# Performance work log

Hardware: AMD Instinct MI355X
Metric: run time of the kernel (lower is better)

Reference implementation:

```python
import jax, jax.numpy as jnp
import numpy as np

NEG = 0.01  # leaky_relu negative slope

def leaky(x):
    return jax.nn.leaky_relu(x, NEG)

def mlp3(x, W0, b0, W1, b1, W2, b2):
    h = leaky(x @ W0 + b0)
    h = leaky(h @ W1 + b1)
    return h @ W2 + b2

B_, T_, N_FINE, F_IN = 2, 4, 64800, 78
N_COARSE, E_LAT, H, D_OUT = 842, 5894, 256, 256

def setup_inputs() -> dict:
    key = jax.random.key(0)
    ks = jax.random.split(key, 24)
    def lin(k, i, o):
        return jax.random.normal(k, (i, o), jnp.float32) * 0.02, jnp.zeros((o,), jnp.float32)
    x = jax.random.normal(ks[0], (B_, T_, N_FINE, F_IN), jnp.float32)
    # one edge per fine node: src = node index, dst = its coarse h3 cell
    edge_index = jnp.stack([jnp.arange(N_FINE, dtype=jnp.int32),
                            jax.random.randint(ks[1], (N_FINE,), 0, N_COARSE, dtype=jnp.int32)])
    edge_attr = 2.0 * jax.random.uniform(ks[2], (N_FINE, 2), jnp.float32) - 1.0  # [sin d, cos d]
    latent_edge_index = jax.random.randint(ks[3], (2, E_LAT), 0, N_COARSE, dtype=jnp.int32)
    latent_edge_attr = 2.0 * jax.random.uniform(ks[4], (E_LAT, 2), jnp.float32) - 1.0
    h3_nodes = jax.random.normal(ks[5], (N_COARSE, F_IN), jnp.float32) * 0.02
    eW0, eb0 = lin(ks[6], 2 * F_IN + 2, H); eW1, eb1 = lin(ks[7], H, H); eW2, eb2 = lin(ks[8], H, D_OUT)
    nW0, nb0 = lin(ks[9], F_IN + D_OUT, H); nW1, nb1 = lin(ks[10], H, H); nW2, nb2 = lin(ks[11], H, D_OUT)
    rW0, rb0 = lin(ks[12], 2, H); rW1, rb1 = lin(ks[13], H, H); rW2, rb2 = lin(ks[14], H, D_OUT)
    rWs, rbs = lin(ks[15], 2, D_OUT)
    return dict(x=x, edge_index=edge_index, edge_attr=edge_attr,
                latent_edge_index=latent_edge_index, latent_edge_attr=latent_edge_attr,
                h3_nodes=h3_nodes,
                eW0=eW0, eb0=eb0, eW1=eW1, eb1=eb1, eW2=eW2, eb2=eb2,
                nW0=nW0, nb0=nb0, nW1=nW1, nb1=nb1, nW2=nW2, nb2=nb2,
                rW0=rW0, rb0=rb0, rW1=rW1, rb1=rb1, rW2=rW2, rb2=rb2,
                rWs=rWs, rbs=rbs)

def reference(x, edge_index, edge_attr, latent_edge_index, latent_edge_attr, h3_nodes,
              eW0, eb0, eW1, eb1, eW2, eb2,
              nW0, nb0, nW1, nb1, nW2, nb2,
              rW0, rb0, rW1, rb1, rW2, rb2, rWs, rbs):
    b, t, n, f = x.shape
    B = b * t
    xf = x.reshape(B, n, f)                      # (b t) n f
    src, dst = edge_index[0], edge_index[1]      # [E]
    nc = h3_nodes.shape[0]
    E = src.shape[0]
    # --- edge MLP: gather src fine feats, dst latent feats, edge attrs ---
    e_in = jnp.concatenate([
        xf[:, src],                                          # [B,E,f]
        jnp.broadcast_to(h3_nodes[dst][None], (B, E, f)),    # [B,E,f]
        jnp.broadcast_to(edge_attr[None], (B, E, 2)),        # [B,E,2]
    ], axis=-1)
    msgs = mlp3(e_in, eW0, eb0, eW1, eb1, eW2, eb2)          # [B,E,D]
    # --- scatter-sum to coarse nodes ---
    agg = jax.vmap(lambda m: jax.ops.segment_sum(m, dst, num_segments=nc))(msgs)  # [B,nc,D]
    # --- node MLP on concat(latent nodes, aggregated messages) ---
    n_in = jnp.concatenate([jnp.broadcast_to(h3_nodes[None], (B, nc, f)), agg], axis=-1)
    nodes = mlp3(n_in, nW0, nb0, nW1, nb1, nW2, nb2)          # [B,nc,D]
    nodes = nodes.reshape(b, t, nc, -1)
    # --- residual MLP over latent edge attrs (eval: dropout off, parametrized skip) ---
    h = leaky(latent_edge_attr @ rW0 + rb0)
    h = leaky(h @ rW1 + rb1)
    attrs = h @ rW2 + rb2 + (latent_edge_attr @ rWs + rbs)
    return (nodes, latent_edge_index, attrs)
```

## Files before the change

### kernel.cpp

```cpp
#include <hip/hip_runtime.h>

#define E_EDGES 64800
#define NC      842
#define NB      8
#define FIN     78
#define E_LAT   5894
#define NROWS_NODE (NB*NC)
#define NTILES_E 2025

#define OUT_IDX_OFF   1724416
#define OUT_IDX_N     11788
#define OUT_ATTR_OFF  1736204

#define AGG_OFF    0
#define CNT_OFF    6897664
#define CUR_OFF    6901032
#define SSRC_OFF   6904400
#define SDST_OFF   7163600
#define SATTR_OFF  7293200
#define WPACK_OFF  7811600

#define WOFF_E0 0
#define WOFF_E1 40960
#define WOFF_E2 106496
#define WOFF_N0 172032
#define WOFF_N1 262144
#define WOFF_N2 327680
#define WOFF_R0 393216
#define WOFF_R1 401408
#define WOFF_R2 466944

#define SH   262
#define SA_N 362

typedef __bf16 bf16x8 __attribute__((ext_vector_type(8)));
typedef float  f32x4  __attribute__((ext_vector_type(4)));

__device__ __forceinline__ unsigned short f2bf(float f) {
    unsigned u = __builtin_bit_cast(unsigned, f);
    return (unsigned short)((u + 0x7fffu + ((u >> 16) & 1u)) >> 16);
}
__device__ __forceinline__ unsigned packRTZ(float lo, float hi) {
    return __builtin_amdgcn_perm(__builtin_bit_cast(unsigned, hi),
                                 __builtin_bit_cast(unsigned, lo), 0x07060302u);
}

template<int MF>
__device__ __forceinline__ void zero_acc(f32x4 (&acc)[MF][4]) {
#pragma unroll
    for (int mf = 0; mf < MF; ++mf)
#pragma unroll
        for (int nf = 0; nf < 4; ++nf)
            acc[mf][nf] = (f32x4){0.f, 0.f, 0.f, 0.f};
}

template<int MF, int NKS>
__device__ __forceinline__ void run_layer(const unsigned short* lA, int strideA,
                                          const unsigned short* Wp, int nfg0,
                                          int m15, int q, f32x4 (&acc)[MF][4]) {
    const unsigned short* wp0 = Wp + (size_t)nfg0 * 512 + (threadIdx.x & 63) * 8;
    bf16x8 bcur[4], bnxt[4];
#pragma unroll
    for (int nf = 0; nf < 4; ++nf) bcur[nf] = *(const bf16x8*)(wp0 + nf * 512);
#pragma unroll
    for (int kk = 0; kk < NKS; ++kk) {
        if (kk + 1 < NKS) {
#pragma unroll
            for (int nf = 0; nf < 4; ++nf)
                bnxt[nf] = *(const bf16x8*)(wp0 + (size_t)(kk + 1) * 16 * 512 + nf * 512);
        }
        bf16x8 a[MF];
#pragma unroll
        for (int mf = 0; mf < MF; ++mf)
            a[mf] = *(const bf16x8*)(lA + (mf * 16 + m15) * strideA + kk * 32 + q * 8);
#pragma unroll
        for (int nf = 0; nf < 4; ++nf)
#pragma unroll
            for (int mf = 0; mf < MF; ++mf)
                acc[mf][nf] = __builtin_amdgcn_mfma_f32_16x16x32_bf16(a[mf], bcur[nf], acc[mf][nf], 0, 0, 0);
#pragma unroll
        for (int nf = 0; nf < 4; ++nf) bcur[nf] = bnxt[nf];
    }
}

template<int MF>
__device__ __forceinline__ void epi_act(unsigned short* Sb, int stride, const f32x4 (&acc)[MF][4],
                                        const float* bias, int w, int m15, int q) {
#pragma unroll
    for (int nf = 0; nf < 4; ++nf) {
        int col = w * 64 + nf * 16 + m15;
        float bv = bias[col];
#pragma unroll
        for (int mf = 0; mf < MF; ++mf)
#pragma unroll
            for (int r4 = 0; r4 < 4; ++r4) {
                int row = mf * 16 + q * 4 + r4;
                float y = acc[mf][nf][r4] + bv;
                y = fmaxf(y, 0.01f * y);
                Sb[row * stride + col] = (unsigned short)(__builtin_bit_cast(unsigned, y) >> 16);
            }
    }
}

__global__ void pack_weights(const float* s0, const float* s1, const float* s2,
                             const float* s3, const float* s4, const float* s5,
                             const float* s6, const float* s7, const float* s8,
                             unsigned short* wp) {
    const int ksA[9]  = {5, 8, 8, 11, 8, 8, 1, 8, 8};
    const int kaA[9]  = {158, 256, 256, 334, 256, 256, 2, 256, 256};
    const int offA[9] = {WOFF_E0, WOFF_E1, WOFF_E2, WOFF_N0, WOFF_N1, WOFF_N2,
                         WOFF_R0, WOFF_R1, WOFF_R2};
    const float* srcs[9] = {s0, s1, s2, s3, s4, s5, s6, s7, s8};
    int rem = blockIdx.x;
    int l = 0;
    while (rem >= ksA[l] * 16) { rem -= ksA[l] * 16; ++l; }
    int kk = rem >> 4, nf = rem & 15;
    int lane = threadIdx.x >> 3, j = threadIdx.x & 7;
    int k = kk * 32 + (lane >> 4) * 8 + j;
    int n = nf * 16 + (lane & 15);
    float v = (k < kaA[l]) ? srcs[l][k * 256 + n] : 0.f;
    wp[(size_t)offA[l] + (size_t)(kk * 16 + nf) * 512 + lane * 8 + j] = f2bf(v);
}

__global__ void hist_kernel(const int* __restrict__ dstA, int* __restrict__ cnt) {
    int e = blockIdx.x * 256 + threadIdx.x;
    if (e < E_EDGES) atomicAdd(&cnt[dstA[e]], 1);
}
__global__ void scan_kernel(const int* __restrict__ cnt, int* __restrict__ cursor) {
    __shared__ int s[1024];
    int t = threadIdx.x;
    s[t] = (t < NC) ? cnt[t] : 0;
    __syncthreads();
    for (int d = 1; d < 1024; d <<= 1) {
        int v = (t >= d) ? s[t - d] : 0;
        __syncthreads();
        s[t] += v;
        __syncthreads();
    }
    if (t < NC) cursor[t] = (t == 0) ? 0 : s[t - 1];
}
__global__ void scatter_kernel(const int* __restrict__ srcA, const int* __restrict__ dstA,
                               const float* __restrict__ eattr, int* __restrict__ cursor,
                               int* __restrict__ ssrc, short* __restrict__ sdst,
                               float2* __restrict__ sattr) {
    int e = blockIdx.x * 256 + threadIdx.x;
    if (e < E_EDGES) {
        int d = dstA[e];
        int p = atomicAdd(&cursor[d], 1);
        ssrc[p] = srcA[e];
        sdst[p] = (short)d;
        sattr[p] = ((const float2*)eattr)[e];
    }
}

__global__ __launch_bounds__(256, 6) void edge_mlp_kernel(
    const float* __restrict__ x, const float* __restrict__ h3,
    const float* __restrict__ eb0, const float* __restrict__ eb1, const float* __restrict__ eb2,
    const unsigned short* __restrict__ wpack, const int* __restrict__ ssrc,
    const short* __restrict__ sdst, const float2* __restrict__ sattr,
    float* __restrict__ agg) {
    __shared__ __align__(16) unsigned short S[32 * SH];
    __shared__ short dstl[32];
    __shared__ unsigned char starts[36];
    __shared__ int nseg;

    const int base = blockIdx.x * 32, b = blockIdx.y;
    const int tid = threadIdx.x, lane = tid & 63, w = tid >> 6;
    const int m15 = lane & 15, q = lane >> 4;

    if (tid < 32) dstl[tid] = sdst[base + tid];
    __syncthreads();

    if (tid == 0) {
        int ns = 0; short prev = -2;
        for (int r = 0; r < 32; ++r) {
            short d = dstl[r];
            if (d != prev) { starts[ns++] = (unsigned char)r; prev = d; }
        }
        starts[ns] = 32;
        nseg = ns;
    }

    {
        const int rr = tid >> 3, j = tid & 7;
        const int eg = base + rr;
        const float* xr = x + ((size_t)b * E_EDGES + ssrc[eg]) * FIN;
        const float* hr = h3 + (int)dstl[rr] * FIN;
        unsigned short* Sr = S + rr * SH;
#pragma unroll
        for (int t = 0; t < 5; ++t) {
            int p = j + 8 * t;
            if (p < 39) {
                float2 f = *(const float2*)(xr + 2 * p);
                float2 g = *(const float2*)(hr + 2 * p);
                *(unsigned*)(Sr + 2 * p) = packRTZ(f.x, f.y);
                *(unsigned*)(Sr + 78 + 2 * p) = packRTZ(g.x, g.y);
            } else if (p == 39) {
                float2 a2 = sattr[eg];
                *(unsigned*)(Sr + 156) = packRTZ(a2.x, a2.y);
                *(unsigned*)(Sr + 158) = 0;
            }
        }
    }
    float bnf[4];
#pragma unroll
    for (int nf = 0; nf < 4; ++nf) bnf[nf] = eb2[w * 64 + nf * 16 + m15];
    __syncthreads();

    f32x4 acc[2][4];
    zero_acc<2>(acc);
    run_layer<2, 5>(S, SH, wpack + WOFF_E0, w * 4, m15, q, acc);
    __syncthreads();
    epi_act<2>(S, SH, acc, eb0, w, m15, q);
    __syncthreads();

    zero_acc<2>(acc);
    run_layer<2, 8>(S, SH, wpack + WOFF_E1, w * 4, m15, q, acc);
    __syncthreads();
    epi_act<2>(S, SH, acc, eb1, w, m15, q);
    __syncthreads();

    zero_acc<2>(acc);
    run_layer<2, 8>(S, SH, wpack + WOFF_E2, w * 4, m15, q, acc);

    const int ns = nseg;
#pragma unroll
    for (int nf = 0; nf < 4; ++nf) {
        for (int s = 0; s < ns; ++s) {
            const int lo = starts[s], hi = starts[s + 1];
            float t = 0.f;
#pragma unroll
            for (int mf = 0; mf < 2; ++mf)
#pragma unroll
                for (int r4 = 0; r4 < 4; ++r4) {
                    int row = mf * 16 + q * 4 + r4;
                    t += (row >= lo && row < hi) ? acc[mf][nf][r4] : 0.f;
                }
            t += __shfl_xor(t, 16, 64);
            t += __shfl_xor(t, 32, 64);
            if (q == nf) {
                int dc = dstl[lo];
                atomicAdd(&agg[((size_t)b * NC + dc) * 256 + w * 64 + nf * 16 + m15],
                          t + bnf[nf] * (float)(hi - lo));
            }
        }
    }
}

__global__ __launch_bounds__(256, 4) void node_mlp_kernel(
    const float* __restrict__ h3, const float* __restrict__ agg,
    const float* __restrict__ nb0, const float* __restrict__ nb1, const float* __restrict__ nb2,
    const unsigned short* __restrict__ wpack, float* __restrict__ out) {
    __shared__ __align__(16) unsigned short S[16 * SA_N];

    const int base = blockIdx.x * 16;
    const int tid = threadIdx.x, lane = tid & 63, w = tid >> 6;
    const int m15 = lane & 15, q = lane >> 4;

    {
        const int rr = tid >> 4, l16 = tid & 15;
        const int jj = base + rr;
        const int vl = jj < NROWS_NODE;
        const int c = vl ? jj % NC : 0;
        const float* hr = h3 + c * FIN;
        const float* ar = agg + (size_t)jj * 256;
        unsigned short* Sr = S + rr * SA_N;
#pragma unroll
        for (int t = 0; t < 12; ++t) {
            int p = l16 + 16 * t;
            if (p < 39) {
                float2 f = *(const float2*)(hr + 2 * p);
                *(unsigned*)(Sr + 2 * p) = packRTZ(f.x, f.y);
            } else if (p < 167) {
                unsigned v = 0;
                if (vl) { float2 f = *(const float2*)(ar + 2 * p - 78); v = packRTZ(f.x, f.y); }
                *(unsigned*)(Sr + 2 * p) = v;
            } else if (p < 176) {
                *(unsigned*)(Sr + 2 * p) = 0;
            }
        }
    }
    __syncthreads();

    f32x4 acc[1][4];
    zero_acc<1>(acc);
    run_layer<1, 11>(S, SA_N, wpack + WOFF_N0, w * 4, m15, q, acc);
    __syncthreads();
    epi_act<1>(S, SA_N, acc, nb0, w, m15, q);
    __syncthreads();

    zero_acc<1>(acc);
    run_layer<1, 8>(S, SA_N, wpack + WOFF_N1, w * 4, m15, q, acc);
    __syncthreads();
    epi_act<1>(S, SA_N, acc, nb1, w, m15, q);
    __syncthreads();

    zero_acc<1>(acc);
    run_layer<1, 8>(S, SA_N, wpack + WOFF_N2, w * 4, m15, q, acc);

#pragma unroll
    for (int nf = 0; nf < 4; ++nf) {
        int col = w * 64 + nf * 16 + m15;
        float bv = nb2[col];
#pragma unroll
        for (int r4 = 0; r4 < 4; ++r4) {
            int jj = base + q * 4 + r4;
            if (jj < NROWS_NODE) out[(size_t)jj * 256 + col] = acc[0][nf][r4] + bv;
        }
    }
}

__global__ __launch_bounds__(256, 4) void tail_kernel(
    const float* __restrict__ la, const float* __restrict__ rb0, const float* __restrict__ rb1,
    const float* __restrict__ rb2, const float* __restrict__ rWs, const float* __restrict__ rbs,
    const unsigned short* __restrict__ wpack, const int* __restrict__ lei,
    float* __restrict__ out) {
    __shared__ __align__(16) unsigned short S[32 * SH];

    const int blk = blockIdx.x;
    const int tid = threadIdx.x;
    if (blk >= 185) {
        for (int i = (blk - 185) * 256 + tid; i < OUT_IDX_N; i += 7 * 256)
            out[OUT_IDX_OFF + i] = (float)lei[i];
        return;
    }

    const int base = blk * 32;
    const int lane = tid & 63, w = tid >> 6;
    const int m15 = lane & 15, q = lane >> 4;

    {
        const int rr = tid >> 3, j = tid & 7;
        unsigned short* Sr = S + rr * SH;
        unsigned v0 = 0;
        if (j == 0 && base + rr < E_LAT) {
            float2 f = *(const float2*)(la + (size_t)(base + rr) * 2);
            v0 = packRTZ(f.x, f.y);
        }
        *(unsigned*)(Sr + 2 * j) = v0;
        *(unsigned*)(Sr + 2 * (j + 8)) = 0;
    }
    __syncthreads();

    f32x4 acc[2][4];
    zero_acc<2>(acc);
    run_layer<2, 1>(S, SH, wpack + WOFF_R0, w * 4, m15, q, acc);
    __syncthreads();
    epi_act<2>(S, SH, acc, rb0, w, m15, q);
    __syncthreads();

    zero_acc<2>(acc);
    run_layer<2, 8>(S, SH, wpack + WOFF_R1, w * 4, m15, q, acc);
    __syncthreads();
    epi_act<2>(S, SH, acc, rb1, w, m15, q);
    __syncthreads();

    zero_acc<2>(acc);
    run_layer<2, 8>(S, SH, wpack + WOFF_R2, w * 4, m15, q, acc);

    float* outA = out + OUT_ATTR_OFF;
#pragma unroll
    for (int nf = 0; nf < 4; ++nf) {
        int col = w * 64 + nf * 16 + m15;
        float bv = rb2[col] + rbs[col];
        float ws0 = rWs[col], ws1 = rWs[256 + col];
#pragma unroll
        for (int mf = 0; mf < 2; ++mf)
#pragma unroll
            for (int r4 = 0; r4 < 4; ++r4) {
                int row = mf * 16 + q * 4 + r4;
                int e = base + row;
                if (e < E_LAT) {
                    float v = acc[mf][nf][r4] + bv + la[e * 2] * ws0 + la[e * 2 + 1] * ws1;
                    outA[(size_t)e * 256 + col] = v;
                }
            }
    }
}

extern "C" void kernel_launch(void* const* d_in, const int* in_sizes, int n_in,
                              void* d_out, int out_size, void* d_ws, size_t ws_size,
                              hipStream_t stream) {
    const float* x      = (const float*)d_in[0];
    const int*   eidx   = (const int*)d_in[1];
    const float* eattr  = (const float*)d_in[2];
    const int*   lei    = (const int*)d_in[3];
    const float* la     = (const float*)d_in[4];
    const float* h3     = (const float*)d_in[5];
    const float* eW0 = (const float*)d_in[6],  *eb0 = (const float*)d_in[7];
    const float* eW1 = (const float*)d_in[8],  *eb1 = (const float*)d_in[9];
    const float* eW2 = (const float*)d_in[10], *eb2 = (const float*)d_in[11];
    const float* nW0 = (const float*)d_in[12], *nb0 = (const float*)d_in[13];
    const float* nW1 = (const float*)d_in[14], *nb1 = (const float*)d_in[15];
    const float* nW2 = (const float*)d_in[16], *nb2 = (const float*)d_in[17];
    const float* rW0 = (const float*)d_in[18], *rb0 = (const float*)d_in[19];
    const float* rW1 = (const float*)d_in[20], *rb1 = (const float*)d_in[21];
    const float* rW2 = (const float*)d_in[22], *rb2 = (const float*)d_in[23];
    const float* rWs = (const float*)d_in[24], *rbs = (const float*)d_in[25];

    char* ws = (char*)d_ws;
    float* agg    = (float*)(ws + AGG_OFF);
    int* cnt      = (int*)(ws + CNT_OFF);
    int* cur      = (int*)(ws + CUR_OFF);
    int* ssrc     = (int*)(ws + SSRC_OFF);
    short* sdst   = (short*)(ws + SDST_OFF);
    float2* sattr = (float2*)(ws + SATTR_OFF);
    unsigned short* wpack = (unsigned short*)(ws + WPACK_OFF);

    float* out = (float*)d_out;

    hipMemsetAsync(d_ws, 0, CUR_OFF, stream);

    pack_weights<<<1040, 512, 0, stream>>>(eW0, eW1, eW2, nW0, nW1, nW2, rW0, rW1, rW2, wpack);
    hist_kernel<<<254, 256, 0, stream>>>(eidx + E_EDGES, cnt);
    scan_kernel<<<1, 1024, 0, stream>>>(cnt, cur);
    scatter_kernel<<<254, 256, 0, stream>>>(eidx, eidx + E_EDGES, eattr, cur,
                                            ssrc, sdst, sattr);
    tail_kernel<<<192, 256, 0, stream>>>(la, rb0, rb1, rb2, rWs, rbs, wpack, lei, out);
    edge_mlp_kernel<<<dim3(NTILES_E, NB), 256, 0, stream>>>(x, h3, eb0, eb1, eb2,
                                                            wpack, ssrc, sdst, sattr, agg);
    node_mlp_kernel<<<421, 256, 0, stream>>>(h3, agg, nb0, nb1, nb2, wpack, out);
}
```

Baseline: 689.8 us.

## Merge sort passes into one block and fold tail MLP into edge kernel

Replaces the histogram, scan and scatter kernels with one single-block kernel that builds the counting sort in shared memory. The residual latent-edge MLP and the index copy now run as extra blocks of the edge MLP grid, with launch bounds raised from 6 to 8 blocks per CU. This cuts kernel launches and the memset of the count buffers, but the counting sort now runs serially on one CU over all 64800 edges. The extra tail blocks launch for every batch slice and most exit at once, and the tighter launch bounds may cause register spills in the edge MLP.

```diff
diff --git a/kernel.cpp b/kernel.cpp
--- a/kernel.cpp
+++ b/kernel.cpp
@@ -7,6 +7,7 @@
 #define E_LAT   5894
 #define NROWS_NODE (NB*NC)
 #define NTILES_E 2025
+#define TAIL_B   192
 
 #define OUT_IDX_OFF   1724416
 #define OUT_IDX_N     11788
@@ -122,51 +123,112 @@
     wp[(size_t)offA[l] + (size_t)(kk * 16 + nf) * 512 + lane * 8 + j] = f2bf(v);
 }
 
-__global__ void hist_kernel(const int* __restrict__ dstA, int* __restrict__ cnt) {
-    int e = blockIdx.x * 256 + threadIdx.x;
-    if (e < E_EDGES) atomicAdd(&cnt[dstA[e]], 1);
-}
-__global__ void scan_kernel(const int* __restrict__ cnt, int* __restrict__ cursor) {
-    __shared__ int s[1024];
-    int t = threadIdx.x;
-    s[t] = (t < NC) ? cnt[t] : 0;
+__global__ __launch_bounds__(1024) void sort_kernel(
+    const int* __restrict__ srcA, const int* __restrict__ dstA,
+    const float* __restrict__ eattr, int* __restrict__ ssrc,
+    short* __restrict__ sdst, float2* __restrict__ sattr) {
+    __shared__ int hist[1024];
+    __shared__ int cur[1024];
+    const int t = threadIdx.x;
+    hist[t] = 0;
+    __syncthreads();
+    for (int e = t; e < E_EDGES; e += 1024) atomicAdd(&hist[dstA[e]], 1);
     __syncthreads();
     for (int d = 1; d < 1024; d <<= 1) {
-        int v = (t >= d) ? s[t - d] : 0;
-        __syncthreads();
-        s[t] += v;
-        __syncthreads();
-    }
-    if (t < NC) cursor[t] = (t == 0) ? 0 : s[t - 1];
-}
-__global__ void scatter_kernel(const int* __restrict__ srcA, const int* __restrict__ dstA,
-                               const float* __restrict__ eattr, int* __restrict__ cursor,
-                               int* __restrict__ ssrc, short* __restrict__ sdst,
-                               float2* __restrict__ sattr) {
-    int e = blockIdx.x * 256 + threadIdx.x;
-    if (e < E_EDGES) {
+        int v = (t >= d) ? hist[t - d] : 0;
+        __syncthreads();
+        hist[t] += v;
+        __syncthreads();
+    }
+    cur[t] = (t == 0) ? 0 : hist[t - 1];
+    __syncthreads();
+    for (int e = t; e < E_EDGES; e += 1024) {
         int d = dstA[e];
-        int p = atomicAdd(&cursor[d], 1);
+        int p = atomicAdd(&cur[d], 1);
         ssrc[p] = srcA[e];
         sdst[p] = (short)d;
         sattr[p] = ((const float2*)eattr)[e];
     }
 }
 
-__global__ __launch_bounds__(256, 6) void edge_mlp_kernel(
+__global__ __launch_bounds__(256, 8) void edge_mlp_kernel(
     const float* __restrict__ x, const float* __restrict__ h3,
     const float* __restrict__ eb0, const float* __restrict__ eb1, const float* __restrict__ eb2,
     const unsigned short* __restrict__ wpack, const int* __restrict__ ssrc,
     const short* __restrict__ sdst, const float2* __restrict__ sattr,
-    float* __restrict__ agg) {
+    float* __restrict__ agg,
+    const float* __restrict__ la, const float* __restrict__ rb0,
+    const float* __restrict__ rb1, const float* __restrict__ rb2,
+    const float* __restrict__ rWs, const float* __restrict__ rbs,
+    const int* __restrict__ lei, float* __restrict__ out) {
     __shared__ __align__(16) unsigned short S[32 * SH];
     __shared__ short dstl[32];
     __shared__ unsigned char starts[36];
     __shared__ int nseg;
 
-    const int base = blockIdx.x * 32, b = blockIdx.y;
     const int tid = threadIdx.x, lane = tid & 63, w = tid >> 6;
     const int m15 = lane & 15, q = lane >> 4;
+
+    if (blockIdx.x >= NTILES_E) {
+        if (blockIdx.y != 0) return;
+        const int blk = blockIdx.x - NTILES_E;
+        if (blk >= 185) {
+            for (int i = (blk - 185) * 256 + tid; i < OUT_IDX_N; i += 7 * 256)
+                out[OUT_IDX_OFF + i] = (float)lei[i];
+            return;
+        }
+        const int base = blk * 32;
+        {
+            const int rr = tid >> 3, j = tid & 7;
+            unsigned short* Sr = S + rr * SH;
+            unsigned v0 = 0;
+            if (j == 0 && base + rr < E_LAT) {
+                float2 f = *(const float2*)(la + (size_t)(base + rr) * 2);
+                v0 = packRTZ(f.x, f.y);
+            }
+            *(unsigned*)(Sr + 2 * j) = v0;
+            *(unsigned*)(Sr + 2 * (j + 8)) = 0;
+        }
+        __syncthreads();
+
+        f32x4 acc[2][4];
+        zero_acc<2>(acc);
+        run_layer<2, 1>(S, SH, wpack + WOFF_R0, w * 4, m15, q, acc);
+        __syncthreads();
+        epi_act<2>(S, SH, acc, rb0, w, m15, q);
+        __syncthreads();
+
+        zero_acc<2>(acc);
+        run_layer<2, 8>(S, SH, wpack + WOFF_R1, w * 4, m15, q, acc);
+        __syncthreads();
+        epi_act<2>(S, SH, acc, rb1, w, m15, q);
+        __syncthreads();
+
+        zero_acc<2>(acc);
+        run_layer<2, 8>(S, SH, wpack + WOFF_R2, w * 4, m15, q, acc);
+
+        float* outA = out + OUT_ATTR_OFF;
+#pragma unroll
+        for (int nf = 0; nf < 4; ++nf) {
+            int col = w * 64 + nf * 16 + m15;
+            float bv = rb2[col] + rbs[col];
+            float ws0 = rWs[col], ws1 = rWs[256 + col];
+#pragma unroll
+            for (int mf = 0; mf < 2; ++mf)
+#pragma unroll
+                for (int r4 = 0; r4 < 4; ++r4) {
+                    int row = mf * 16 + q * 4 + r4;
+                    int e = base + row;
+                    if (e < E_LAT) {
+                        float v = acc[mf][nf][r4] + bv + la[e * 2] * ws0 + la[e * 2 + 1] * ws1;
+                        outA[(size_t)e * 256 + col] = v;
+                    }
+                }
+        }
+        return;
+    }
+
+    const int base = blockIdx.x * 32, b = blockIdx.y;
 
     if (tid < 32) dstl[tid] = sdst[base + tid];
     __syncthreads();
@@ -307,74 +369,6 @@
             int jj = base + q * 4 + r4;
             if (jj < NROWS_NODE) out[(size_t)jj * 256 + col] = acc[0][nf][r4] + bv;
         }
-    }
-}
-
-__global__ __launch_bounds__(256, 4) void tail_kernel(
-    const float* __restrict__ la, const float* __restrict__ rb0, const float* __restrict__ rb1,
-    const float* __restrict__ rb2, const float* __restrict__ rWs, const float* __restrict__ rbs,
-    const unsigned short* __restrict__ wpack, const int* __restrict__ lei,
-    float* __restrict__ out) {
-    __shared__ __align__(16) unsigned short S[32 * SH];
-
-    const int blk = blockIdx.x;
-    const int tid = threadIdx.x;
-    if (blk >= 185) {
-        for (int i = (blk - 185) * 256 + tid; i < OUT_IDX_N; i += 7 * 256)
-            out[OUT_IDX_OFF + i] = (float)lei[i];
-        return;
-    }
-
-    const int base = blk * 32;
-    const int lane = tid & 63, w = tid >> 6;
-    const int m15 = lane & 15, q = lane >> 4;
-
-    {
-        const int rr = tid >> 3, j = tid & 7;
-        unsigned short* Sr = S + rr * SH;
-        unsigned v0 = 0;
-        if (j == 0 && base + rr < E_LAT) {
-            float2 f = *(const float2*)(la + (size_t)(base + rr) * 2);
-            v0 = packRTZ(f.x, f.y);
-        }
-        *(unsigned*)(Sr + 2 * j) = v0;
-        *(unsigned*)(Sr + 2 * (j + 8)) = 0;
-    }
-    __syncthreads();
-
-    f32x4 acc[2][4];
-    zero_acc<2>(acc);
-    run_layer<2, 1>(S, SH, wpack + WOFF_R0, w * 4, m15, q, acc);
-    __syncthreads();
-    epi_act<2>(S, SH, acc, rb0, w, m15, q);
-    __syncthreads();
-
-    zero_acc<2>(acc);
-    run_layer<2, 8>(S, SH, wpack + WOFF_R1, w * 4, m15, q, acc);
-    __syncthreads();
-    epi_act<2>(S, SH, acc, rb1, w, m15, q);
-    __syncthreads();
-
-    zero_acc<2>(acc);
-    run_layer<2, 8>(S, SH, wpack + WOFF_R2, w * 4, m15, q, acc);
-
-    float* outA = out + OUT_ATTR_OFF;
-#pragma unroll
-    for (int nf = 0; nf < 4; ++nf) {
-        int col = w * 64 + nf * 16 + m15;
-        float bv = rb2[col] + rbs[col];
-        float ws0 = rWs[col], ws1 = rWs[256 + col];
-#pragma unroll
-        for (int mf = 0; mf < 2; ++mf)
-#pragma unroll
-            for (int r4 = 0; r4 < 4; ++r4) {
-                int row = mf * 16 + q * 4 + r4;
-                int e = base + row;
-                if (e < E_LAT) {
-                    float v = acc[mf][nf][r4] + bv + la[e * 2] * ws0 + la[e * 2 + 1] * ws1;
-                    outA[(size_t)e * 256 + col] = v;
-                }
-            }
     }
 }
 
@@ -400,8 +394,6 @@
 
     char* ws = (char*)d_ws;
     float* agg    = (float*)(ws + AGG_OFF);
-    int* cnt      = (int*)(ws + CNT_OFF);
-    int* cur      = (int*)(ws + CUR_OFF);
     int* ssrc     = (int*)(ws + SSRC_OFF);
     short* sdst   = (short*)(ws + SDST_OFF);
     float2* sattr = (float2*)(ws + SATTR_OFF);
@@ -409,15 +401,12 @@
 
     float* out = (float*)d_out;
 
-    hipMemsetAsync(d_ws, 0, CUR_OFF, stream);
+    hipMemsetAsync(d_ws, 0, CNT_OFF, stream);
 
     pack_weights<<<1040, 512, 0, stream>>>(eW0, eW1, eW2, nW0, nW1, nW2, rW0, rW1, rW2, wpack);
-    hist_kernel<<<254, 256, 0, stream>>>(eidx + E_EDGES, cnt);
-    scan_kernel<<<1, 1024, 0, stream>>>(cnt, cur);
-    scatter_kernel<<<254, 256, 0, stream>>>(eidx, eidx + E_EDGES, eattr, cur,
-                                            ssrc, sdst, sattr);
-    tail_kernel<<<192, 256, 0, stream>>>(la, rb0, rb1, rb2, rWs, rbs, wpack, lei, out);
-    edge_mlp_kernel<<<dim3(NTILES_E, NB), 256, 0, stream>>>(x, h3, eb0, eb1, eb2,
-                                                            wpack, ssrc, sdst, sattr, agg);
+    sort_kernel<<<1, 1024, 0, stream>>>(eidx, eidx + E_EDGES, eattr, ssrc, sdst, sattr);
+    edge_mlp_kernel<<<dim3(NTILES_E + TAIL_B, NB), 256, 0, stream>>>(
+        x, h3, eb0, eb1, eb2, wpack, ssrc, sdst, sattr, agg,
+        la, rb0, rb1, rb2, rWs, rbs, lei, out);
     node_mlp_kernel<<<421, 256, 0, stream>>>(h3, agg, nb0, nb1, nb2, wpack, out);
 }
```

Measured after the change: 889.8 us. 1.29x slower.

## Batch all eight timesteps per edge tile and fold tail MLP into edge kernel

Applied to the files above, without the earlier changes.

Each edge block now takes 16 sorted edges across all 8 batch slices, giving 128 rows, instead of 32 edges for a single batch slice. Each weight fragment loaded per MFMA step is therefore reused over four times as many rows, and the segment bookkeeping and index loads are shared across batches. The latent-edge tail MLP is merged into the same launch as extra blocks, removing one kernel launch. In exchange the accumulator grows to 8x4 fragments and shared memory to 128 rows, so launch bounds drop to 2 blocks per CU, which may hurt occupancy or cause register spills.

```diff
diff --git a/kernel.cpp b/kernel.cpp
--- a/kernel.cpp
+++ b/kernel.cpp
@@ -6,7 +6,9 @@
 #define FIN     78
 #define E_LAT   5894
 #define NROWS_NODE (NB*NC)
-#define NTILES_E 2025
+#define EPB      16
+#define NTILES_E 4050
+#define TAIL_B   192
 
 #define OUT_IDX_OFF   1724416
 #define OUT_IDX_N     11788
@@ -153,52 +155,123 @@
     }
 }
 
-__global__ __launch_bounds__(256, 6) void edge_mlp_kernel(
+__global__ __launch_bounds__(256, 2) void edge_mlp_kernel(
     const float* __restrict__ x, const float* __restrict__ h3,
     const float* __restrict__ eb0, const float* __restrict__ eb1, const float* __restrict__ eb2,
     const unsigned short* __restrict__ wpack, const int* __restrict__ ssrc,
     const short* __restrict__ sdst, const float2* __restrict__ sattr,
-    float* __restrict__ agg) {
-    __shared__ __align__(16) unsigned short S[32 * SH];
-    __shared__ short dstl[32];
-    __shared__ unsigned char starts[36];
+    float* __restrict__ agg,
+    const float* __restrict__ la, const float* __restrict__ rb0,
+    const float* __restrict__ rb1, const float* __restrict__ rb2,
+    const float* __restrict__ rWs, const float* __restrict__ rbs,
+    const int* __restrict__ lei, float* __restrict__ out) {
+    __shared__ __align__(16) unsigned short S[128 * SH];
+    __shared__ short dstl[EPB];
+    __shared__ int   srcl[EPB];
+    __shared__ unsigned char starts[EPB + 4];
     __shared__ int nseg;
 
-    const int base = blockIdx.x * 32, b = blockIdx.y;
     const int tid = threadIdx.x, lane = tid & 63, w = tid >> 6;
     const int m15 = lane & 15, q = lane >> 4;
 
-    if (tid < 32) dstl[tid] = sdst[base + tid];
+    if (blockIdx.x >= NTILES_E) {
+        const int blk = blockIdx.x - NTILES_E;
+        if (blk >= 185) {
+            for (int i = (blk - 185) * 256 + tid; i < OUT_IDX_N; i += 7 * 256)
+                out[OUT_IDX_OFF + i] = (float)lei[i];
+            return;
+        }
+        const int base = blk * 32;
+        {
+            const int rr = tid >> 3, j = tid & 7;
+            unsigned short* Sr = S + rr * SH;
+            unsigned v0 = 0;
+            if (j == 0 && base + rr < E_LAT) {
+                float2 f = *(const float2*)(la + (size_t)(base + rr) * 2);
+                v0 = packRTZ(f.x, f.y);
+            }
+            *(unsigned*)(Sr + 2 * j) = v0;
+            *(unsigned*)(Sr + 2 * (j + 8)) = 0;
+        }
+        __syncthreads();
+
+        f32x4 acc[2][4];
+        zero_acc<2>(acc);
+        run_layer<2, 1>(S, SH, wpack + WOFF_R0, w * 4, m15, q, acc);
+        __syncthreads();
+        epi_act<2>(S, SH, acc, rb0, w, m15, q);
+        __syncthreads();
+
+        zero_acc<2>(acc);
+        run_layer<2, 8>(S, SH, wpack + WOFF_R1, w * 4, m15, q, acc);
+        __syncthreads();
+        epi_act<2>(S, SH, acc, rb1, w, m15, q);
+        __syncthreads();
+
+        zero_acc<2>(acc);
+        run_layer<2, 8>(S, SH, wpack + WOFF_R2, w * 4, m15, q, acc);
+
+        float* outA = out + OUT_ATTR_OFF;
+#pragma unroll
+        for (int nf = 0; nf < 4; ++nf) {
+            int col = w * 64 + nf * 16 + m15;
+            float bv = rb2[col] + rbs[col];
+            float ws0 = rWs[col], ws1 = rWs[256 + col];
+#pragma unroll
+            for (int mf = 0; mf < 2; ++mf)
+#pragma unroll
+                for (int r4 = 0; r4 < 4; ++r4) {
+                    int row = mf * 16 + q * 4 + r4;
+                    int e = base + row;
+                    if (e < E_LAT) {
+                        float v = acc[mf][nf][r4] + bv + la[e * 2] * ws0 + la[e * 2 + 1] * ws1;
+                        outA[(size_t)e * 256 + col] = v;
+                    }
+                }
+        }
+        return;
+    }
+
+    const int base = blockIdx.x * EPB;
+
+    if (tid < EPB) {
+        dstl[tid] = sdst[base + tid];
+        srcl[tid] = ssrc[base + tid];
+    }
     __syncthreads();
 
     if (tid == 0) {
         int ns = 0; short prev = -2;
-        for (int r = 0; r < 32; ++r) {
+        for (int r = 0; r < EPB; ++r) {
             short d = dstl[r];
             if (d != prev) { starts[ns++] = (unsigned char)r; prev = d; }
         }
-        starts[ns] = 32;
+        starts[ns] = EPB;
         nseg = ns;
     }
 
     {
         const int rr = tid >> 3, j = tid & 7;
-        const int eg = base + rr;
-        const float* xr = x + ((size_t)b * E_EDGES + ssrc[eg]) * FIN;
-        const float* hr = h3 + (int)dstl[rr] * FIN;
-        unsigned short* Sr = S + rr * SH;
-#pragma unroll
-        for (int t = 0; t < 5; ++t) {
-            int p = j + 8 * t;
-            if (p < 39) {
-                float2 f = *(const float2*)(xr + 2 * p);
-                float2 g = *(const float2*)(hr + 2 * p);
-                *(unsigned*)(Sr + 2 * p) = packRTZ(f.x, f.y);
-                *(unsigned*)(Sr + 78 + 2 * p) = packRTZ(g.x, g.y);
-            } else if (p == 39) {
-                float2 a2 = sattr[eg];
-                *(unsigned*)(Sr + 156) = packRTZ(a2.x, a2.y);
-                *(unsigned*)(Sr + 158) = 0;
+#pragma unroll
+        for (int pass = 0; pass < 4; ++pass) {
+            const int row = pass * 32 + rr;
+            const int b = row >> 4, e = row & 15;
+            const float* xr = x + ((size_t)b * E_EDGES + srcl[e]) * FIN;
+            const float* hr = h3 + (int)dstl[e] * FIN;
+            unsigned short* Sr = S + row * SH;
+#pragma unroll
+            for (int t = 0; t < 5; ++t) {
+                int p = j + 8 * t;
+                if (p < 39) {
+                    float2 f = *(const float2*)(xr + 2 * p);
+                    float2 g = *(const float2*)(hr + 2 * p);
+                    *(unsigned*)(Sr + 2 * p) = packRTZ(f.x, f.y);
+                    *(unsigned*)(Sr + 78 + 2 * p) = packRTZ(g.x, g.y);
+                } else if (p == 39) {
+                    float2 a2 = sattr[base + e];
+                    *(unsigned*)(Sr + 156) = packRTZ(a2.x, a2.y);
+                    *(unsigned*)(Sr + 158) = 0;
+                }
             }
         }
     }
@@ -207,41 +280,42 @@
     for (int nf = 0; nf < 4; ++nf) bnf[nf] = eb2[w * 64 + nf * 16 + m15];
     __syncthreads();
 
-    f32x4 acc[2][4];
-    zero_acc<2>(acc);
-    run_layer<2, 5>(S, SH, wpack + WOFF_E0, w * 4, m15, q, acc);
-    __syncthreads();
-    epi_act<2>(S, SH, acc, eb0, w, m15, q);
-    __syncthreads();
-
-    zero_acc<2>(acc);
-    run_layer<2, 8>(S, SH, wpack + WOFF_E1, w * 4, m15, q, acc);
-    __syncthreads();
-    epi_act<2>(S, SH, acc, eb1, w, m15, q);
-    __syncthreads();
-
-    zero_acc<2>(acc);
-    run_layer<2, 8>(S, SH, wpack + WOFF_E2, w * 4, m15, q, acc);
+    f32x4 acc[8][4];
+    zero_acc<8>(acc);
+    run_layer<8, 5>(S, SH, wpack + WOFF_E0, w * 4, m15, q, acc);
+    __syncthreads();
+    epi_act<8>(S, SH, acc, eb0, w, m15, q);
+    __syncthreads();
+
+    zero_acc<8>(acc);
+    run_layer<8, 8>(S, SH, wpack + WOFF_E1, w * 4, m15, q, acc);
+    __syncthreads();
+    epi_act<8>(S, SH, acc, eb1, w, m15, q);
+    __syncthreads();
+
+    zero_acc<8>(acc);
+    run_layer<8, 8>(S, SH, wpack + WOFF_E2, w * 4, m15, q, acc);
 
     const int ns = nseg;
 #pragma unroll
     for (int nf = 0; nf < 4; ++nf) {
         for (int s = 0; s < ns; ++s) {
             const int lo = starts[s], hi = starts[s + 1];
-            float t = 0.f;
-#pragma unroll
-            for (int mf = 0; mf < 2; ++mf)
+            const int dc = dstl[lo];
+#pragma unroll
+            for (int mf = 0; mf < 8; ++mf) {
+                float t = 0.f;
 #pragma unroll
                 for (int r4 = 0; r4 < 4; ++r4) {
-                    int row = mf * 16 + q * 4 + r4;
-                    t += (row >= lo && row < hi) ? acc[mf][nf][r4] : 0.f;
+                    int e = q * 4 + r4;
+                    t += (e >= lo && e < hi) ? acc[mf][nf][r4] : 0.f;
                 }
-            t += __shfl_xor(t, 16, 64);
-            t += __shfl_xor(t, 32, 64);
-            if (q == nf) {
-                int dc = dstl[lo];
-                atomicAdd(&agg[((size_t)b * NC + dc) * 256 + w * 64 + nf * 16 + m15],
-                          t + bnf[nf] * (float)(hi - lo));
+                t += __shfl_xor(t, 16, 64);
+                t += __shfl_xor(t, 32, 64);
+                if (q == nf) {
+                    atomicAdd(&agg[((size_t)mf * NC + dc) * 256 + w * 64 + nf * 16 + m15],
+                              t + bnf[nf] * (float)(hi - lo));
+                }
             }
         }
     }
@@ -307,74 +381,6 @@
             int jj = base + q * 4 + r4;
             if (jj < NROWS_NODE) out[(size_t)jj * 256 + col] = acc[0][nf][r4] + bv;
         }
-    }
-}
-
-__global__ __launch_bounds__(256, 4) void tail_kernel(
-    const float* __restrict__ la, const float* __restrict__ rb0, const float* __restrict__ rb1,
-    const float* __restrict__ rb2, const float* __restrict__ rWs, const float* __restrict__ rbs,
-    const unsigned short* __restrict__ wpack, const int* __restrict__ lei,
-    float* __restrict__ out) {
-    __shared__ __align__(16) unsigned short S[32 * SH];
-
-    const int blk = blockIdx.x;
-    const int tid = threadIdx.x;
-    if (blk >= 185) {
-        for (int i = (blk - 185) * 256 + tid; i < OUT_IDX_N; i += 7 * 256)
-            out[OUT_IDX_OFF + i] = (float)lei[i];
-        return;
-    }
-
-    const int base = blk * 32;
-    const int lane = tid & 63, w = tid >> 6;
-    const int m15 = lane & 15, q = lane >> 4;
-
-    {
-        const int rr = tid >> 3, j = tid & 7;
-        unsigned short* Sr = S + rr * SH;
-        unsigned v0 = 0;
-        if (j == 0 && base + rr < E_LAT) {
-            float2 f = *(const float2*)(la + (size_t)(base + rr) * 2);
-            v0 = packRTZ(f.x, f.y);
-        }
-        *(unsigned*)(Sr + 2 * j) = v0;
-        *(unsigned*)(Sr + 2 * (j + 8)) = 0;
-    }
-    __syncthreads();
-
-    f32x4 acc[2][4];
-    zero_acc<2>(acc);
-    run_layer<2, 1>(S, SH, wpack + WOFF_R0, w * 4, m15, q, acc);
-    __syncthreads();
-    epi_act<2>(S, SH, acc, rb0, w, m15, q);
-    __syncthreads();
-
-    zero_acc<2>(acc);
-    run_layer<2, 8>(S, SH, wpack + WOFF_R1, w * 4, m15, q, acc);
-    __syncthreads();
-    epi_act<2>(S, SH, acc, rb1, w, m15, q);
-    __syncthreads();
-
-    zero_acc<2>(acc);
-    run_layer<2, 8>(S, SH, wpack + WOFF_R2, w * 4, m15, q, acc);
-
-    float* outA = out + OUT_ATTR_OFF;
-#pragma unroll
-    for (int nf = 0; nf < 4; ++nf) {
-        int col = w * 64 + nf * 16 + m15;
-        float bv = rb2[col] + rbs[col];
-        float ws0 = rWs[col], ws1 = rWs[256 + col];
-#pragma unroll
-        for (int mf = 0; mf < 2; ++mf)
-#pragma unroll
-            for (int r4 = 0; r4 < 4; ++r4) {
-                int row = mf * 16 + q * 4 + r4;
-                int e = base + row;
-                if (e < E_LAT) {
-                    float v = acc[mf][nf][r4] + bv + la[e * 2] * ws0 + la[e * 2 + 1] * ws1;
-                    outA[(size_t)e * 256 + col] = v;
-                }
-            }
     }
 }
 
@@ -416,8 +422,8 @@
     scan_kernel<<<1, 1024, 0, stream>>>(cnt, cur);
     scatter_kernel<<<254, 256, 0, stream>>>(eidx, eidx + E_EDGES, eattr, cur,
                                             ssrc, sdst, sattr);
-    tail_kernel<<<192, 256, 0, stream>>>(la, rb0, rb1, rb2, rWs, rbs, wpack, lei, out);
-    edge_mlp_kernel<<<dim3(NTILES_E, NB), 256, 0, stream>>>(x, h3, eb0, eb1, eb2,
-                                                            wpack, ssrc, sdst, sattr, agg);
+    edge_mlp_kernel<<<NTILES_E + TAIL_B, 256, 0, stream>>>(
+        x, h3, eb0, eb1, eb2, wpack, ssrc, sdst, sattr, agg,
+        la, rb0, rb1, rb2, rWs, rbs, lei, out);
     node_mlp_kernel<<<421, 256, 0, stream>>>(h3, agg, nb0, nb1, nb2, wpack, out);
 }
```

Result: slower. 733.0 us (+6.3%).

## Precompute h3 projection of first edge layer and merge tail into node kernel

Applied to the files above, without the earlier changes.

The h3_nodes part of the first edge-MLP layer is now computed once per coarse node (842x256) by a small fp32 kernel and added in the layer-0 epilogue by a gather on dst, so the edge MMA K dimension drops from 160 to 96. The precomputed table is parked in the output's attrs region, which is later overwritten by the tail work. The tail kernel is merged into the node kernel launch so it runs after the edge kernel. This removes per-edge h3 loads and about 40% of layer-0 MMA work, at the cost of a gathered fp32 read per row in the epilogue and putting the tail work on the critical path.

```diff
diff --git a/kernel.cpp b/kernel.cpp
--- a/kernel.cpp
+++ b/kernel.cpp
@@ -7,6 +7,8 @@
 #define E_LAT   5894
 #define NROWS_NODE (NB*NC)
 #define NTILES_E 2025
+#define NODE_B   421
+#define TAIL_B   192
 
 #define OUT_IDX_OFF   1724416
 #define OUT_IDX_N     11788
@@ -21,14 +23,14 @@
 #define WPACK_OFF  7811600
 
 #define WOFF_E0 0
-#define WOFF_E1 40960
-#define WOFF_E2 106496
-#define WOFF_N0 172032
-#define WOFF_N1 262144
-#define WOFF_N2 327680
-#define WOFF_R0 393216
-#define WOFF_R1 401408
-#define WOFF_R2 466944
+#define WOFF_E1 24576
+#define WOFF_E2 90112
+#define WOFF_N0 155648
+#define WOFF_N1 245760
+#define WOFF_N2 311296
+#define WOFF_R0 376832
+#define WOFF_R1 385024
+#define WOFF_R2 450560
 
 #define SH   262
 #define SA_N 362
@@ -106,8 +108,8 @@
                              const float* s3, const float* s4, const float* s5,
                              const float* s6, const float* s7, const float* s8,
                              unsigned short* wp) {
-    const int ksA[9]  = {5, 8, 8, 11, 8, 8, 1, 8, 8};
-    const int kaA[9]  = {158, 256, 256, 334, 256, 256, 2, 256, 256};
+    const int ksA[9]  = {3, 8, 8, 11, 8, 8, 1, 8, 8};
+    const int kaA[9]  = {96, 256, 256, 334, 256, 256, 2, 256, 256};
     const int offA[9] = {WOFF_E0, WOFF_E1, WOFF_E2, WOFF_N0, WOFF_N1, WOFF_N2,
                          WOFF_R0, WOFF_R1, WOFF_R2};
     const float* srcs[9] = {s0, s1, s2, s3, s4, s5, s6, s7, s8};
@@ -118,8 +120,43 @@
     int lane = threadIdx.x >> 3, j = threadIdx.x & 7;
     int k = kk * 32 + (lane >> 4) * 8 + j;
     int n = nf * 16 + (lane & 15);
-    float v = (k < kaA[l]) ? srcs[l][k * 256 + n] : 0.f;
+    float v = 0.f;
+    if (l == 0) {
+        int sr = (k < 78) ? k : ((k < 80) ? 156 + (k - 78) : -1);
+        if (sr >= 0) v = s0[sr * 256 + n];
+    } else {
+        v = (k < kaA[l]) ? srcs[l][k * 256 + n] : 0.f;
+    }
     wp[(size_t)offA[l] + (size_t)(kk * 16 + nf) * 512 + lane * 8 + j] = f2bf(v);
+}
+
+__global__ __launch_bounds__(256) void h3mm_kernel(const float* __restrict__ h3,
+                                                   const float* __restrict__ eW0,
+                                                   const float* __restrict__ eb0,
+                                                   float* __restrict__ h3we) {
+    __shared__ float hs[16][80];
+    const int tid = threadIdx.x;
+    const int rbase = blockIdx.x * 16;
+    for (int i = tid; i < 16 * 78; i += 256) {
+        int r = i / 78, k = i % 78;
+        int gr = rbase + r;
+        hs[r][k] = (gr < NC) ? h3[gr * FIN + k] : 0.f;
+    }
+    __syncthreads();
+    const int c = tid;
+    float acc[16];
+#pragma unroll
+    for (int r = 0; r < 16; ++r) acc[r] = eb0[c];
+    for (int k = 0; k < 78; ++k) {
+        float wv = eW0[(78 + k) * 256 + c];
+#pragma unroll
+        for (int r = 0; r < 16; ++r) acc[r] = fmaf(hs[r][k], wv, acc[r]);
+    }
+#pragma unroll
+    for (int r = 0; r < 16; ++r) {
+        int gr = rbase + r;
+        if (gr < NC) h3we[(size_t)gr * 256 + c] = acc[r];
+    }
 }
 
 __global__ void hist_kernel(const int* __restrict__ dstA, int* __restrict__ cnt) {
@@ -154,8 +191,8 @@
 }
 
 __global__ __launch_bounds__(256, 6) void edge_mlp_kernel(
-    const float* __restrict__ x, const float* __restrict__ h3,
-    const float* __restrict__ eb0, const float* __restrict__ eb1, const float* __restrict__ eb2,
+    const float* __restrict__ x, const float* __restrict__ h3we,
+    const float* __restrict__ eb1, const float* __restrict__ eb2,
     const unsigned short* __restrict__ wpack, const int* __restrict__ ssrc,
     const short* __restrict__ sdst, const float2* __restrict__ sattr,
     float* __restrict__ agg) {
@@ -185,20 +222,18 @@
         const int rr = tid >> 3, j = tid & 7;
         const int eg = base + rr;
         const float* xr = x + ((size_t)b * E_EDGES + ssrc[eg]) * FIN;
-        const float* hr = h3 + (int)dstl[rr] * FIN;
         unsigned short* Sr = S + rr * SH;
 #pragma unroll
-        for (int t = 0; t < 5; ++t) {
+        for (int t = 0; t < 6; ++t) {
             int p = j + 8 * t;
             if (p < 39) {
                 float2 f = *(const float2*)(xr + 2 * p);
-                float2 g = *(const float2*)(hr + 2 * p);
                 *(unsigned*)(Sr + 2 * p) = packRTZ(f.x, f.y);
-                *(unsigned*)(Sr + 78 + 2 * p) = packRTZ(g.x, g.y);
             } else if (p == 39) {
                 float2 a2 = sattr[eg];
-                *(unsigned*)(Sr + 156) = packRTZ(a2.x, a2.y);
-                *(unsigned*)(Sr + 158) = 0;
+                *(unsigned*)(Sr + 78) = packRTZ(a2.x, a2.y);
+            } else {
+                *(unsigned*)(Sr + 2 * p) = 0;
             }
         }
     }
@@ -209,9 +244,24 @@
 
     f32x4 acc[2][4];
     zero_acc<2>(acc);
-    run_layer<2, 5>(S, SH, wpack + WOFF_E0, w * 4, m15, q, acc);
-    __syncthreads();
-    epi_act<2>(S, SH, acc, eb0, w, m15, q);
+    run_layer<2, 3>(S, SH, wpack + WOFF_E0, w * 4, m15, q, acc);
+    __syncthreads();
+    {
+#pragma unroll
+        for (int mf = 0; mf < 2; ++mf)
+#pragma unroll
+            for (int r4 = 0; r4 < 4; ++r4) {
+                int row = mf * 16 + q * 4 + r4;
+                const float* hb = h3we + (size_t)dstl[row] * 256;
+#pragma unroll
+                for (int nf = 0; nf < 4; ++nf) {
+                    int col = w * 64 + nf * 16 + m15;
+                    float y = acc[mf][nf][r4] + hb[col];
+                    y = fmaxf(y, 0.01f * y);
+                    S[row * SH + col] = (unsigned short)(__builtin_bit_cast(unsigned, y) >> 16);
+                }
+            }
+    }
     __syncthreads();
 
     zero_acc<2>(acc);
@@ -247,15 +297,78 @@
     }
 }
 
-__global__ __launch_bounds__(256, 4) void node_mlp_kernel(
+__global__ __launch_bounds__(256, 4) void node_tail_kernel(
     const float* __restrict__ h3, const float* __restrict__ agg,
     const float* __restrict__ nb0, const float* __restrict__ nb1, const float* __restrict__ nb2,
-    const unsigned short* __restrict__ wpack, float* __restrict__ out) {
-    __shared__ __align__(16) unsigned short S[16 * SA_N];
-
-    const int base = blockIdx.x * 16;
+    const unsigned short* __restrict__ wpack, float* __restrict__ out,
+    const float* __restrict__ la, const float* __restrict__ rb0,
+    const float* __restrict__ rb1, const float* __restrict__ rb2,
+    const float* __restrict__ rWs, const float* __restrict__ rbs,
+    const int* __restrict__ lei) {
+    __shared__ __align__(16) unsigned short S[32 * SH];
+
     const int tid = threadIdx.x, lane = tid & 63, w = tid >> 6;
     const int m15 = lane & 15, q = lane >> 4;
+
+    if (blockIdx.x >= NODE_B) {
+        const int blk = blockIdx.x - NODE_B;
+        if (blk >= 185) {
+            for (int i = (blk - 185) * 256 + tid; i < OUT_IDX_N; i += 7 * 256)
+                out[OUT_IDX_OFF + i] = (float)lei[i];
+            return;
+        }
+        const int base = blk * 32;
+        {
+            const int rr = tid >> 3, jj = tid & 7;
+            unsigned short* Sr = S + rr * SH;
+            unsigned v0 = 0;
+            if (jj == 0 && base + rr < E_LAT) {
+                float2 f = *(const float2*)(la + (size_t)(base + rr) * 2);
+                v0 = packRTZ(f.x, f.y);
+            }
+            *(unsigned*)(Sr + 2 * jj) = v0;
+            *(unsigned*)(Sr + 2 * (jj + 8)) = 0;
+        }
+        __syncthreads();
+
+        f32x4 acc[2][4];
+        zero_acc<2>(acc);
+        run_layer<2, 1>(S, SH, wpack + WOFF_R0, w * 4, m15, q, acc);
+        __syncthreads();
+        epi_act<2>(S, SH, acc, rb0, w, m15, q);
+        __syncthreads();
+
+        zero_acc<2>(acc);
+        run_layer<2, 8>(S, SH, wpack + WOFF_R1, w * 4, m15, q, acc);
+        __syncthreads();
+        epi_act<2>(S, SH, acc, rb1, w, m15, q);
+        __syncthreads();
+
+        zero_acc<2>(acc);
+        run_layer<2, 8>(S, SH, wpack + WOFF_R2, w * 4, m15, q, acc);
+
+        float* outA = out + OUT_ATTR_OFF;
+#pragma unroll
+        for (int nf = 0; nf < 4; ++nf) {
+            int col = w * 64 + nf * 16 + m15;
+            float bv = rb2[col] + rbs[col];
+            float ws0 = rWs[col], ws1 = rWs[256 + col];
+#pragma unroll
+            for (int mf = 0; mf < 2; ++mf)
+#pragma unroll
+                for (int r4 = 0; r4 < 4; ++r4) {
+                    int row = mf * 16 + q * 4 + r4;
+                    int e = base + row;
+                    if (e < E_LAT) {
+                        float v = acc[mf][nf][r4] + bv + la[e * 2] * ws0 + la[e * 2 + 1] * ws1;
+                        outA[(size_t)e * 256 + col] = v;
+                    }
+                }
+        }
+        return;
+    }
+
+    const int base = blockIdx.x * 16;
 
     {
         const int rr = tid >> 4, l16 = tid & 15;
@@ -266,8 +379,8 @@
         const float* ar = agg + (size_t)jj * 256;
         unsigned short* Sr = S + rr * SA_N;
 #pragma unroll
-        for (int t = 0; t < 12; ++t) {
-            int p = l16 + 16 * t;
+        for (int tt = 0; tt < 12; ++tt) {
+            int p = l16 + 16 * tt;
             if (p < 39) {
                 float2 f = *(const float2*)(hr + 2 * p);
                 *(unsigned*)(Sr + 2 * p) = packRTZ(f.x, f.y);
@@ -307,74 +420,6 @@
             int jj = base + q * 4 + r4;
             if (jj < NROWS_NODE) out[(size_t)jj * 256 + col] = acc[0][nf][r4] + bv;
         }
-    }
-}
-
-__global__ __launch_bounds__(256, 4) void tail_kernel(
-    const float* __restrict__ la, const float* __restrict__ rb0, const float* __restrict__ rb1,
-    const float* __restrict__ rb2, const float* __restrict__ rWs, const float* __restrict__ rbs,
-    const unsigned short* __restrict__ wpack, const int* __restrict__ lei,
-    float* __restrict__ out) {
-    __shared__ __align__(16) unsigned short S[32 * SH];
-
-    const int blk = blockIdx.x;
-    const int tid = threadIdx.x;
-    if (blk >= 185) {
-        for (int i = (blk - 185) * 256 + tid; i < OUT_IDX_N; i += 7 * 256)
-            out[OUT_IDX_OFF + i] = (float)lei[i];
-        return;
-    }
-
-    const int base = blk * 32;
-    const int lane = tid & 63, w = tid >> 6;
-    const int m15 = lane & 15, q = lane >> 4;
-
-    {
-        const int rr = tid >> 3, j = tid & 7;
-        unsigned short* Sr = S + rr * SH;
-        unsigned v0 = 0;
-        if (j == 0 && base + rr < E_LAT) {
-            float2 f = *(const float2*)(la + (size_t)(base + rr) * 2);
-            v0 = packRTZ(f.x, f.y);
-        }
-        *(unsigned*)(Sr + 2 * j) = v0;
-        *(unsigned*)(Sr + 2 * (j + 8)) = 0;
-    }
-    __syncthreads();
-
-    f32x4 acc[2][4];
-    zero_acc<2>(acc);
-    run_layer<2, 1>(S, SH, wpack + WOFF_R0, w * 4, m15, q, acc);
-    __syncthreads();
-    epi_act<2>(S, SH, acc, rb0, w, m15, q);
-    __syncthreads();
-
-    zero_acc<2>(acc);
-    run_layer<2, 8>(S, SH, wpack + WOFF_R1, w * 4, m15, q, acc);
-    __syncthreads();
-    epi_act<2>(S, SH, acc, rb1, w, m15, q);
-    __syncthreads();
-
-    zero_acc<2>(acc);
-    run_layer<2, 8>(S, SH, wpack + WOFF_R2, w * 4, m15, q, acc);
-
-    float* outA = out + OUT_ATTR_OFF;
-#pragma unroll
-    for (int nf = 0; nf < 4; ++nf) {
-        int col = w * 64 + nf * 16 + m15;
-        float bv = rb2[col] + rbs[col];
-        float ws0 = rWs[col], ws1 = rWs[256 + col];
-#pragma unroll
-        for (int mf = 0; mf < 2; ++mf)
-#pragma unroll
-            for (int r4 = 0; r4 < 4; ++r4) {
-                int row = mf * 16 + q * 4 + r4;
-                int e = base + row;
-                if (e < E_LAT) {
-                    float v = acc[mf][nf][r4] + bv + la[e * 2] * ws0 + la[e * 2 + 1] * ws1;
-                    outA[(size_t)e * 256 + col] = v;
-                }
-            }
     }
 }
 
@@ -408,16 +453,19 @@
     unsigned short* wpack = (unsigned short*)(ws + WPACK_OFF);
 
     float* out = (float*)d_out;
+    float* h3we = out + OUT_ATTR_OFF;
 
     hipMemsetAsync(d_ws, 0, CUR_OFF, stream);
 
-    pack_weights<<<1040, 512, 0, stream>>>(eW0, eW1, eW2, nW0, nW1, nW2, rW0, rW1, rW2, wpack);
+    pack_weights<<<1008, 512, 0, stream>>>(eW0, eW1, eW2, nW0, nW1, nW2, rW0, rW1, rW2, wpack);
+    h3mm_kernel<<<53, 256, 0, stream>>>(h3, eW0, eb0, h3we);
     hist_kernel<<<254, 256, 0, stream>>>(eidx + E_EDGES, cnt);
     scan_kernel<<<1, 1024, 0, stream>>>(cnt, cur);
     scatter_kernel<<<254, 256, 0, stream>>>(eidx, eidx + E_EDGES, eattr, cur,
                                             ssrc, sdst, sattr);
-    tail_kernel<<<192, 256, 0, stream>>>(la, rb0, rb1, rb2, rWs, rbs, wpack, lei, out);
-    edge_mlp_kernel<<<dim3(NTILES_E, NB), 256, 0, stream>>>(x, h3, eb0, eb1, eb2,
+    edge_mlp_kernel<<<dim3(NTILES_E, NB), 256, 0, stream>>>(x, h3we, eb1, eb2,
                                                             wpack, ssrc, sdst, sattr, agg);
-    node_mlp_kernel<<<421, 256, 0, stream>>>(h3, agg, nb0, nb1, nb2, wpack, out);
-}
+    node_tail_kernel<<<NODE_B + TAIL_B, 256, 0, stream>>>(
+        h3, agg, nb0, nb1, nb2, wpack, out,
+        la, rb0, rb1, rb2, rWs, rbs, lei);
+}
```

Result: no change. 677.4 us (-1.8%).
